# Performance work log

Measured on AMD Instinct MI355X. Metric: run time of the kernel, lower is better.

Reference implementation:

```python
import jax, jax.numpy as jnp
import numpy as np

FORGET_BIAS = 1.0  # TF LSTMCell default

def _lstm_step(c, h, x, W, b):
    # TF BasicLSTM/LSTMCell gate order: i, j (cell candidate), f, o
    z = jnp.concatenate([x, h], axis=-1) @ W + b
    i, j, f, o = jnp.split(z, 4, axis=-1)
    c_new = c * jax.nn.sigmoid(f + FORGET_BIAS) + jax.nn.sigmoid(i) * jnp.tanh(j)
    h_new = jnp.tanh(c_new) * jax.nn.sigmoid(o)
    return c_new, h_new

def setup_inputs() -> dict:
    key = jax.random.key(0)
    k1, k2, k3 = jax.random.split(key, 3)
    B, T, D, H1, H2 = 512, 2048, 1, 64, 1
    x = jax.random.normal(k1, (B, T, D), dtype=jnp.float32)
    W1 = jax.random.normal(k2, (D + H1, 4 * H1), dtype=jnp.float32) * 0.1
    b1 = jnp.zeros((4 * H1,), dtype=jnp.float32)
    W2 = jax.random.normal(k3, (H1 + H2, 4 * H2), dtype=jnp.float32) * 0.1
    b2 = jnp.zeros((4 * H2,), dtype=jnp.float32)
    return {"x": x, "W1": W1, "b1": b1, "W2": W2, "b2": b2}

def reference(x, W1, b1, W2, b2):
    B = x.shape[0]
    H1 = W1.shape[1] // 4
    H2 = W2.shape[1] // 4
    init = (jnp.zeros((B, H1), x.dtype), jnp.zeros((B, H1), x.dtype),
            jnp.zeros((B, H2), x.dtype), jnp.zeros((B, H2), x.dtype))

    def step(carry, x_t):
        c1, h1, c2, h2 = carry
        c1, h1 = _lstm_step(c1, h1, x_t, W1, b1)   # layer 1: LSTMCell(64)
        c2, h2 = _lstm_step(c2, h2, h1, W2, b2)    # layer 2: LSTMCell(1)
        return (c1, h1, c2, h2), h2

    xs = jnp.swapaxes(x, 0, 1)           # [T, B, 1]
    _, ys = jax.lax.scan(step, init, xs)  # ys: [T, B, 1]
    return jnp.swapaxes(ys, 0, 1)         # [B, T, 1]
```

## Files before the change

### kernel.cpp

```cpp
#include <hip/hip_runtime.h>

#define TT 2048

typedef float v2f __attribute__((ext_vector_type(2)));
typedef _Float16 h2v __attribute__((ext_vector_type(2)));

__device__ __forceinline__ v2f mk2(float a, float b) { v2f r; r.x = a; r.y = b; return r; }
__device__ __forceinline__ float rcpf(float x) { return __builtin_amdgcn_rcpf(x); }
__device__ __forceinline__ float fsig(float x) { return rcpf(1.0f + __expf(-x)); }
__device__ __forceinline__ float ftanh(float x) {
    return fmaf(2.0f, rcpf(1.0f + __expf(-2.0f * x)), -1.0f);
}

template<int C>
__device__ __forceinline__ float dppmov(float s) {
    return __int_as_float(__builtin_amdgcn_update_dpp(
        __float_as_int(s), __float_as_int(s), C, 0xF, 0xF, false));
}
template<int Q>
__device__ __forceinline__ float qbcast(float x) {
    return __int_as_float(__builtin_amdgcn_update_dpp(
        __float_as_int(x), __float_as_int(x), Q * 0x55, 0xF, 0xF, false));
}

#if __has_builtin(__builtin_amdgcn_fdot2)
#define DOT2(a, b, c) __builtin_amdgcn_fdot2((a), (b), (c), false)
#else
#define DOT2(a, b, c) fmaf((float)(a).x, (float)(b).x, \
                      fmaf((float)(a).y, (float)(b).y, (c)))
#endif

__device__ __forceinline__ h2v pk2(float a, float b) {
#if __has_builtin(__builtin_amdgcn_cvt_pkrtz)
    return __builtin_bit_cast(h2v, __builtin_amdgcn_cvt_pkrtz(a, b));
#else
    h2v r; r.x = (_Float16)a; r.y = (_Float16)b; return r;
#endif
}
__device__ __forceinline__ h2v bch(int v) { return __builtin_bit_cast(h2v, v); }

__global__ __launch_bounds__(64)
__attribute__((amdgpu_waves_per_eu(2, 2)))
void lstm1_f16(const float* __restrict__ x,
               const float* __restrict__ W1,
               const float* __restrict__ b1,
               const float* __restrict__ W2,
               float* __restrict__ zout)
{
    __shared__ __align__(16) float xall[TT];
    __shared__ __align__(16) _Float16 hring[16 * 72];
    __shared__ __align__(16) int wF4[8][64][4];
    __shared__ __align__(16) int wO4[8][64][4];
    __shared__ __align__(16) _Float16 w2lds[4][72];

    const int lane = threadIdx.x & 63;
    const int e    = blockIdx.x;
    const int u    = lane;

    for (int i = lane; i < TT; i += 64) xall[i] = x[(size_t)e * TT + i];
    for (int i = lane; i < 576; i += 64) ((int*)hring)[i] = 0;
    for (int kp = 0; kp < 32; ++kp) {
        wF4[kp >> 2][u][kp & 3] = __builtin_bit_cast(int,
            pk2(W1[(1 + 2*kp)*256 + 128 + u], W1[(2 + 2*kp)*256 + 128 + u]));
        wO4[kp >> 2][u][kp & 3] = __builtin_bit_cast(int,
            pk2(W1[(1 + 2*kp)*256 + 192 + u], W1[(2 + 2*kp)*256 + 192 + u]));
    }
    w2lds[0][lane] = (_Float16)W2[lane * 4 + 0];
    w2lds[1][lane] = (_Float16)W2[lane * 4 + 1];
    w2lds[2][lane] = (_Float16)W2[lane * 4 + 2];
    w2lds[3][lane] = (_Float16)W2[lane * 4 + 3];

#define DWQ(G, GO, q) \
    const h2v w##G##q##x = pk2(W1[(1+8*(q))*256 + (GO)*64 + u], W1[(2+8*(q))*256 + (GO)*64 + u]); \
    const h2v w##G##q##y = pk2(W1[(3+8*(q))*256 + (GO)*64 + u], W1[(4+8*(q))*256 + (GO)*64 + u]); \
    const h2v w##G##q##z = pk2(W1[(5+8*(q))*256 + (GO)*64 + u], W1[(6+8*(q))*256 + (GO)*64 + u]); \
    const h2v w##G##q##w = pk2(W1[(7+8*(q))*256 + (GO)*64 + u], W1[(8+8*(q))*256 + (GO)*64 + u]);
    DWQ(I, 0, 0) DWQ(I, 0, 1) DWQ(I, 0, 2) DWQ(I, 0, 3)
    DWQ(I, 0, 4) DWQ(I, 0, 5) DWQ(I, 0, 6) DWQ(I, 0, 7)
    DWQ(J, 1, 0) DWQ(J, 1, 1) DWQ(J, 1, 2) DWQ(J, 1, 3)
    DWQ(J, 1, 4) DWQ(J, 1, 5) DWQ(J, 1, 6) DWQ(J, 1, 7)
#undef DWQ

    const float w0I = W1[u],        bI = b1[u];
    const float w0J = W1[64 + u],   bJ = b1[64 + u];
    const float w0F = W1[128 + u],  bF = b1[128 + u] + 1.0f;
    const float w0O = W1[192 + u],  bO = b1[192 + u];

    const int tl = lane >> 2, gq = lane & 3;

    float c1 = 0.0f;
    __syncthreads();

    float* __restrict__ zb = zout + (size_t)e * TT * 4;
    const int* __restrict__ wFb = &wF4[0][0][0] + (u << 2);
    const int* __restrict__ wOb = &wO4[0][0][0] + (u << 2);

#define DGIJ(S, q, v) \
    accI##S = DOT2(bch((v).x), wI##q##x, accI##S); \
    accJ##S = DOT2(bch((v).x), wJ##q##x, accJ##S); \
    accI##S = DOT2(bch((v).y), wI##q##y, accI##S); \
    accJ##S = DOT2(bch((v).y), wJ##q##y, accJ##S); \
    accI##S = DOT2(bch((v).z), wI##q##z, accI##S); \
    accJ##S = DOT2(bch((v).z), wJ##q##z, accJ##S); \
    accI##S = DOT2(bch((v).w), wI##q##w, accI##S); \
    accJ##S = DOT2(bch((v).w), wJ##q##w, accJ##S);
#define FOD4(S, g, qv) { \
    const int4 wf_ = *(const int4*)(wFb + (g) * 256); \
    const int4 wo_ = *(const int4*)(wOb + (g) * 256); \
    accF##S = DOT2(bch((qv).x), bch(wf_.x), accF##S); \
    accO##S = DOT2(bch((qv).x), bch(wo_.x), accO##S); \
    accF##S = DOT2(bch((qv).y), bch(wf_.y), accF##S); \
    accO##S = DOT2(bch((qv).y), bch(wo_.y), accO##S); \
    accF##S = DOT2(bch((qv).z), bch(wf_.z), accF##S); \
    accO##S = DOT2(bch((qv).z), bch(wo_.z), accO##S); \
    accF##S = DOT2(bch((qv).w), bch(wf_.w), accF##S); \
    accO##S = DOT2(bch((qv).w), bch(wo_.w), accO##S); \
}

    for (int t = 0; t < TT; ++t) {
        const int4* hp = (const int4*)&hring[((t - 1) & 15) * 72];
        const int4 q0 = hp[0], q1 = hp[1], q2 = hp[2], q3 = hp[3];
        const int4 q4 = hp[4], q5 = hp[5], q6 = hp[6], q7 = hp[7];
        float accI0 = bI, accJ0 = bJ, accF0 = bF, accO0 = bO;
        float accI1 = 0.f, accJ1 = 0.f, accF1 = 0.f, accO1 = 0.f;
        DGIJ(0, 0, q0) DGIJ(1, 4, q4)
        DGIJ(0, 1, q1) DGIJ(1, 5, q5)
        DGIJ(0, 2, q2) DGIJ(1, 6, q6)
        DGIJ(0, 3, q3) DGIJ(1, 7, q7)
        FOD4(0, 0, q0) FOD4(1, 4, q4)
        FOD4(0, 1, q1) FOD4(1, 5, q5)
        FOD4(0, 2, q2) FOD4(1, 6, q6)
        FOD4(0, 3, q3) FOD4(1, 7, q7)
        const float xt = xall[t];
        const float zI = fmaf(xt, w0I, accI0 + accI1);
        const float zJ = fmaf(xt, w0J, accJ0 + accJ1);
        const float zF = fmaf(xt, w0F, accF0 + accF1);
        const float zO = fmaf(xt, w0O, accO0 + accO1);
        const float i_ = fsig(zI);
        const float j_ = ftanh(zJ);
        const float f_ = fsig(zF);
        const float o_ = fsig(zO);
        c1 = fmaf(c1, f_, i_ * j_);
        const float h1 = ftanh(c1) * o_;
        hring[(t & 15) * 72 + u] = (_Float16)h1;

        if ((t & 15) == 15) {
            const int4* hb  = (const int4*)&hring[tl * 72];
            const int4* w2q = (const int4*)&w2lds[gq][0];
            float z2 = 0.0f;
#pragma unroll
            for (int q = 0; q < 8; ++q) {
                const int4 wv = w2q[q];
                const int4 va = hb[q];
                z2 = DOT2(bch(va.x), bch(wv.x), z2);
                z2 = DOT2(bch(va.y), bch(wv.y), z2);
                z2 = DOT2(bch(va.z), bch(wv.z), z2);
                z2 = DOT2(bch(va.w), bch(wv.w), z2);
            }
            zb[(size_t)(t - 15 + tl) * 4 + gq] = z2;
        }
    }
#undef DGIJ
#undef FOD4
}

__global__ __launch_bounds__(64)
void lstm2_chain(const float* __restrict__ zp,
                 const float* __restrict__ W2,
                 const float* __restrict__ b2,
                 float* __restrict__ out)
{
    const int lane = threadIdx.x & 63;
    const int e    = lane >> 2;
    const int g    = lane & 3;
    const int elem = (blockIdx.x << 4) + e;

    const float w2h = W2[256 + g];
    const float bb  = b2[g] + ((g == 2) ? 1.0f : 0.0f);
    const float nlm = (g == 1) ? -2.0f : -1.0f;
    const float k2  = (g == 1) ?  2.0f :  1.0f;
    const float k3  = (g == 1) ? -1.0f :  0.0f;

    const float* __restrict__ zrow = zp + (size_t)elem * TT * 4 + g;
    float* __restrict__ orow = out + (size_t)elem * TT;

    float c2 = 0.0f, h2 = 0.0f;

    float zc[16];
#pragma unroll
    for (int k = 0; k < 16; ++k) zc[k] = zrow[k << 2];

    for (int t0 = 0; t0 < TT; t0 += 16) {
        float zn[16];
        if (t0 + 16 < TT) {
#pragma unroll
            for (int k = 0; k < 16; ++k) zn[k] = zrow[((t0 + 16 + k) << 2)];
        }
        float st0 = 0.f, st1 = 0.f, st2 = 0.f, st3 = 0.f;
#pragma unroll
        for (int k = 0; k < 16; ++k) {
            const float arg = fmaf(w2h, h2, zc[k] + bb);
            const float ev  = __expf(arg * nlm);
            const float rv  = rcpf(1.0f + ev);
            const float v   = fmaf(k2, rv, k3);
            const float vi = qbcast<0>(v), vj = qbcast<1>(v);
            const float vf = qbcast<2>(v), vo = qbcast<3>(v);
            c2 = fmaf(c2, vf, vi * vj);
            h2 = ftanh(c2) * vo;
            const bool mine = (g == (k & 3));
            if ((k >> 2) == 0) st0 = mine ? h2 : st0;
            else if ((k >> 2) == 1) st1 = mine ? h2 : st1;
            else if ((k >> 2) == 2) st2 = mine ? h2 : st2;
            else st3 = mine ? h2 : st3;
        }
        orow[t0 + g]      = st0;
        orow[t0 + 4 + g]  = st1;
        orow[t0 + 8 + g]  = st2;
        orow[t0 + 12 + g] = st3;
#pragma unroll
        for (int k = 0; k < 16; ++k) zc[k] = zn[k];
    }
}

__global__ __launch_bounds__(512)
__attribute__((amdgpu_waves_per_eu(4, 4)))
void lstm2_mono(const float* __restrict__ x,
                const float* __restrict__ W1,
                const float* __restrict__ b1,
                const float* __restrict__ W2,
                const float* __restrict__ b2,
                float* __restrict__ out)
{
    __shared__ __align__(16) float xall[TT + 4];
    __shared__ __align__(16) float h1x[2][80];
    __shared__ __align__(16) float zpq[4][4];
    __shared__ __align__(16) float h2buf[2][64];

    const int tid  = threadIdx.x;
    const int wave = tid >> 6;
    const int lane = tid & 63;
    const int b    = blockIdx.x;

    for (int i = tid; i < TT; i += 512) xall[i] = x[b * TT + i];
    if (tid < 4) xall[TT + tid] = 0.0f;

    const int u    = lane >> 3;
    const int h    = (lane >> 2) & 1;
    const int g    = lane & 3;
    const int unit = (wave << 3) + u;
    const int col  = (g << 6) + unit;

#define DECLW(k) const v2f wq##k = mk2(W1[(1 + 32*h + 2*(k)) * 256 + col], \
                                       W1[(2 + 32*h + 2*(k)) * 256 + col]);
    DECLW(0)  DECLW(1)  DECLW(2)  DECLW(3)
    DECLW(4)  DECLW(5)  DECLW(6)  DECLW(7)
    DECLW(8)  DECLW(9)  DECLW(10) DECLW(11)
    DECLW(12) DECLW(13) DECLW(14) DECLW(15)
#undef DECLW

    const float w0x   = (h == 0) ? W1[col] : 0.0f;
    const float biasF = (h == 0) ? (b1[col] + ((g == 2) ? 1.0f : 0.0f)) : 0.0f;
    const float nlm   = (g == 1) ? -2.0f : -1.0f;
    const bool  isj   = (g == 1);

    const float w2g  = W2[lane * 4 + (wave & 3)];
    const float w2h0 = W2[256], w2h1 = W2[257], w2h2 = W2[258], w2h3 = W2[259];
    const float b20 = b2[0], b21 = b2[1], b22 = b2[2], b23 = b2[3];

    float c1 = 0.0f;
    float c2 = 0.0f, h2v2 = 0.0f;

    const int hbase = h * 48;
    const int ridx  = lane + ((lane >> 5) << 4);
    const int widx  = (unit < 32) ? unit : unit + 16;

    if (tid < 160) ((float*)h1x)[tid] = 0.0f;
    __syncthreads();

    float* __restrict__ outb = out + b * TT;

#define WSUM(s) ({ float _s = (s);                                            \
    _s += dppmov<0x111>(_s); _s += dppmov<0x112>(_s); _s += dppmov<0x114>(_s);\
    _s += dppmov<0x118>(_s); _s += dppmov<0x142>(_s); _s += dppmov<0x143>(_s);\
    _s; })

#define STEP(P, t, xv)                                                        \
    {                                                                         \
        if ((t) < TT) {                                                       \
            const float4* hp = (const float4*)&h1x[P][hbase];                 \
            const float4 q0 = hp[0], q1 = hp[1], q2 = hp[2], q3 = hp[3];      \
            const float4 q4 = hp[4], q5 = hp[5], q6 = hp[6], q7 = hp[7];      \
            v2f a0 = mk2(fmaf((xv), w0x, biasF), 0.0f);                       \
            v2f a1 = mk2(0.f, 0.f), a2 = mk2(0.f, 0.f), a3 = mk2(0.f, 0.f);  \
            a0 = __builtin_elementwise_fma(mk2(q0.x, q0.y), wq0,  a0);        \
            a1 = __builtin_elementwise_fma(mk2(q0.z, q0.w), wq1,  a1);        \
            a2 = __builtin_elementwise_fma(mk2(q1.x, q1.y), wq2,  a2);        \
            a3 = __builtin_elementwise_fma(mk2(q1.z, q1.w), wq3,  a3);        \
            a0 = __builtin_elementwise_fma(mk2(q2.x, q2.y), wq4,  a0);        \
            a1 = __builtin_elementwise_fma(mk2(q2.z, q2.w), wq5,  a1);        \
            a2 = __builtin_elementwise_fma(mk2(q3.x, q3.y), wq6,  a2);        \
            a3 = __builtin_elementwise_fma(mk2(q3.z, q3.w), wq7,  a3);        \
            a0 = __builtin_elementwise_fma(mk2(q4.x, q4.y), wq8,  a0);        \
            a1 = __builtin_elementwise_fma(mk2(q4.z, q4.w), wq9,  a1);        \
            a2 = __builtin_elementwise_fma(mk2(q5.x, q5.y), wq10, a2);        \
            a3 = __builtin_elementwise_fma(mk2(q5.z, q5.w), wq11, a3);        \
            a0 = __builtin_elementwise_fma(mk2(q6.x, q6.y), wq12, a0);        \
            a1 = __builtin_elementwise_fma(mk2(q6.z, q6.w), wq13, a1);        \
            a2 = __builtin_elementwise_fma(mk2(q7.x, q7.y), wq14, a2);        \
            a3 = __builtin_elementwise_fma(mk2(q7.z, q7.w), wq15, a3);        \
            const v2f sv = (a0 + a1) + (a2 + a3);                             \
            const float zh = sv.x + sv.y;                                     \
            const float tshr = dppmov<0x114>(zh);                             \
            const float tshl = dppmov<0x104>(zh);                             \
            const float zfull = zh + (h ? tshr : tshl);                       \
            const float e = __expf(zfull * nlm);                              \
            const float r = rcpf(1.0f + e);                                   \
            const float v = isj ? fmaf(2.0f, r, -1.0f) : r;                   \
            const float gi = qbcast<0>(v), gj = qbcast<1>(v);                 \
            const float gf = qbcast<2>(v), go = qbcast<3>(v);                 \
            c1 = fmaf(c1, gf, gi * gj);                                       \
            const float h1v = ftanh(c1) * go;                                 \
            if ((lane & 7) == 0) h1x[(P) ^ 1][widx] = h1v;                    \
        }                                                                     \
        if (wave < 4 && (t) >= 1 && (t) <= TT) {                              \
            const float s = WSUM(h1x[P][ridx] * w2g);                         \
            if (lane == 63) zpq[((t) - 1) & 3][wave] = s;                     \
        }                                                                     \
        if (wave == 7 && lane == 0 && (t) >= 2 && (t) <= TT + 1) {            \
            const int st = (t) - 2;                                           \
            const float4 z4 = *(const float4*)zpq[st & 3];                    \
            const float zi = z4.x + fmaf(h2v2, w2h0, b20);                    \
            const float zj = z4.y + fmaf(h2v2, w2h1, b21);                    \
            const float zf = z4.z + fmaf(h2v2, w2h2, b22);                    \
            const float zo = z4.w + fmaf(h2v2, w2h3, b23);                    \
            c2 = c2 * fsig(zf + 1.0f) + fsig(zi) * ftanh(zj);                 \
            h2v2 = ftanh(c2) * fsig(zo);                                      \
            h2buf[(st >> 6) & 1][st & 63] = h2v2;                             \
        }                                                                     \
        __syncthreads();                                                      \
        if (wave == 4 && (t) >= 66 && ((t) & 63) == 2) {                      \
            const int blk = ((t) - 66) >> 6;                                  \
            outb[(blk << 6) + lane] = h2buf[blk & 1][lane];                   \
        }                                                                     \
    }

    for (int it = 0; it <= TT + 2; it += 2) {
        const float2 x2 = *(const float2*)&xall[it];
        STEP(0, it,     x2.x)
        STEP(1, it + 1, x2.y)
    }
#undef STEP
#undef WSUM
}

extern "C" void kernel_launch(void* const* d_in, const int* in_sizes, int n_in,
                              void* d_out, int out_size, void* d_ws, size_t ws_size,
                              hipStream_t stream)
{
    const float* x  = (const float*)d_in[0];
    const float* W1 = (const float*)d_in[1];
    const float* b1 = (const float*)d_in[2];
    const float* W2 = (const float*)d_in[3];
    const float* b2 = (const float*)d_in[4];
    float* out = (float*)d_out;

    const size_t need = (size_t)512 * TT * 4 * sizeof(float);
    if (ws_size >= need) {
        float* zp = (float*)d_ws;
        lstm1_f16<<<512, 64, 0, stream>>>(x, W1, b1, W2, zp);
        lstm2_chain<<<512 / 16, 64, 0, stream>>>(zp, W2, b2, out);
    } else {
        lstm2_mono<<<512, 512, 0, stream>>>(x, W1, b1, W2, b2, out);
    }
}
```

Measured before the change: 1.051 ms.

## Compute F/O gate recurrent dot products with MFMA, keep I/J on packed dot2

Moves the forget and output gate recurrent matvec (64x128) from per-lane fdot2 with LDS weight loads onto 16x16x32 f16 MFMA instructions. The weights are re-laid out in LDS as B fragments, and h is broadcast as the A operand, so only row 0 of each 16-row tile is useful. The I and J gates stay on register-resident fdot2. The waves-per-EU hint is also relaxed. The aim is to split the work between the matrix and vector units within each timestep. The cost is wasted MFMA rows, MFMA latency on the serial recurrence, and extra select logic to pick each lane's result.

```diff
diff --git a/kernel.cpp b/kernel.cpp
--- a/kernel.cpp
+++ b/kernel.cpp
@@ -4,6 +4,8 @@
 
 typedef float v2f __attribute__((ext_vector_type(2)));
 typedef _Float16 h2v __attribute__((ext_vector_type(2)));
+typedef _Float16 f16x8 __attribute__((ext_vector_type(8)));
+typedef float f32x4 __attribute__((ext_vector_type(4)));
 
 __device__ __forceinline__ v2f mk2(float a, float b) { v2f r; r.x = a; r.y = b; return r; }
 __device__ __forceinline__ float rcpf(float x) { return __builtin_amdgcn_rcpf(x); }
@@ -40,8 +42,8 @@
 __device__ __forceinline__ h2v bch(int v) { return __builtin_bit_cast(h2v, v); }
 
 __global__ __launch_bounds__(64)
-__attribute__((amdgpu_waves_per_eu(2, 2)))
-void lstm1_f16(const float* __restrict__ x,
+__attribute__((amdgpu_waves_per_eu(1)))
+void lstm1_hyb(const float* __restrict__ x,
                const float* __restrict__ W1,
                const float* __restrict__ b1,
                const float* __restrict__ W2,
@@ -49,22 +51,22 @@
 {
     __shared__ __align__(16) float xall[TT];
     __shared__ __align__(16) _Float16 hring[16 * 72];
-    __shared__ __align__(16) int wF4[8][64][4];
-    __shared__ __align__(16) int wO4[8][64][4];
+    __shared__ __align__(16) _Float16 wfo[2][8][64][8];
     __shared__ __align__(16) _Float16 w2lds[4][72];
 
     const int lane = threadIdx.x & 63;
     const int e    = blockIdx.x;
     const int u    = lane;
+    const int lg   = lane >> 4;
 
     for (int i = lane; i < TT; i += 64) xall[i] = x[(size_t)e * TT + i];
     for (int i = lane; i < 576; i += 64) ((int*)hring)[i] = 0;
-    for (int kp = 0; kp < 32; ++kp) {
-        wF4[kp >> 2][u][kp & 3] = __builtin_bit_cast(int,
-            pk2(W1[(1 + 2*kp)*256 + 128 + u], W1[(2 + 2*kp)*256 + 128 + u]));
-        wO4[kp >> 2][u][kp & 3] = __builtin_bit_cast(int,
-            pk2(W1[(1 + 2*kp)*256 + 192 + u], W1[(2 + 2*kp)*256 + 192 + u]));
-    }
+    for (int kt = 0; kt < 2; ++kt)
+        for (int n8 = 0; n8 < 8; ++n8)
+#pragma unroll
+            for (int j = 0; j < 8; ++j)
+                wfo[kt][n8][u][j] = (_Float16)
+                    W1[(size_t)(1 + kt*32 + (u >> 4)*8 + j) * 256 + 128 + 16*n8 + (u & 15)];
     w2lds[0][lane] = (_Float16)W2[lane * 4 + 0];
     w2lds[1][lane] = (_Float16)W2[lane * 4 + 1];
     w2lds[2][lane] = (_Float16)W2[lane * 4 + 2];
@@ -92,8 +94,7 @@
     __syncthreads();
 
     float* __restrict__ zb = zout + (size_t)e * TT * 4;
-    const int* __restrict__ wFb = &wF4[0][0][0] + (u << 2);
-    const int* __restrict__ wOb = &wO4[0][0][0] + (u << 2);
+    const f32x4 zf = {0.0f, 0.0f, 0.0f, 0.0f};
 
 #define DGIJ(S, q, v) \
     accI##S = DOT2(bch((v).x), wI##q##x, accI##S); \
@@ -104,40 +105,41 @@
     accJ##S = DOT2(bch((v).z), wJ##q##z, accJ##S); \
     accI##S = DOT2(bch((v).w), wI##q##w, accI##S); \
     accJ##S = DOT2(bch((v).w), wJ##q##w, accJ##S);
-#define FOD4(S, g, qv) { \
-    const int4 wf_ = *(const int4*)(wFb + (g) * 256); \
-    const int4 wo_ = *(const int4*)(wOb + (g) * 256); \
-    accF##S = DOT2(bch((qv).x), bch(wf_.x), accF##S); \
-    accO##S = DOT2(bch((qv).x), bch(wo_.x), accO##S); \
-    accF##S = DOT2(bch((qv).y), bch(wf_.y), accF##S); \
-    accO##S = DOT2(bch((qv).y), bch(wo_.y), accO##S); \
-    accF##S = DOT2(bch((qv).z), bch(wf_.z), accF##S); \
-    accO##S = DOT2(bch((qv).z), bch(wo_.z), accO##S); \
-    accF##S = DOT2(bch((qv).w), bch(wf_.w), accF##S); \
-    accO##S = DOT2(bch((qv).w), bch(wo_.w), accO##S); \
-}
+
+#define MM(a, b, c) __builtin_amdgcn_mfma_f32_16x16x32_f16((a), (b), (c), 0, 0, 0)
+#define LB(kt, n8) (*(const f16x8*)(&wfo[(kt)][(n8)][0][0] + (u << 3) + boff))
 
     for (int t = 0; t < TT; ++t) {
-        const int4* hp = (const int4*)&hring[((t - 1) & 15) * 72];
+        int boff = 0; asm volatile("" : "+v"(boff));
+        const int slot = ((t - 1) & 15) * 72;
+        const f16x8 A0 = *(const f16x8*)&hring[slot + lg * 8];
+        const f16x8 A1 = *(const f16x8*)&hring[slot + 32 + lg * 8];
+        const int4* hp = (const int4*)&hring[slot];
         const int4 q0 = hp[0], q1 = hp[1], q2 = hp[2], q3 = hp[3];
         const int4 q4 = hp[4], q5 = hp[5], q6 = hp[6], q7 = hp[7];
-        float accI0 = bI, accJ0 = bJ, accF0 = bF, accO0 = bO;
-        float accI1 = 0.f, accJ1 = 0.f, accF1 = 0.f, accO1 = 0.f;
+        f32x4 acF0 = MM(A0, LB(0,0), zf), acF1 = MM(A0, LB(0,1), zf);
+        f32x4 acF2 = MM(A0, LB(0,2), zf), acF3 = MM(A0, LB(0,3), zf);
+        f32x4 acO0 = MM(A0, LB(0,4), zf), acO1 = MM(A0, LB(0,5), zf);
+        f32x4 acO2 = MM(A0, LB(0,6), zf), acO3 = MM(A0, LB(0,7), zf);
+        acF0 = MM(A1, LB(1,0), acF0); acF1 = MM(A1, LB(1,1), acF1);
+        acF2 = MM(A1, LB(1,2), acF2); acF3 = MM(A1, LB(1,3), acF3);
+        acO0 = MM(A1, LB(1,4), acO0); acO1 = MM(A1, LB(1,5), acO1);
+        acO2 = MM(A1, LB(1,6), acO2); acO3 = MM(A1, LB(1,7), acO3);
+        float accI0 = bI, accJ0 = bJ;
+        float accI1 = 0.f, accJ1 = 0.f;
         DGIJ(0, 0, q0) DGIJ(1, 4, q4)
         DGIJ(0, 1, q1) DGIJ(1, 5, q5)
         DGIJ(0, 2, q2) DGIJ(1, 6, q6)
         DGIJ(0, 3, q3) DGIJ(1, 7, q7)
-        FOD4(0, 0, q0) FOD4(1, 4, q4)
-        FOD4(0, 1, q1) FOD4(1, 5, q5)
-        FOD4(0, 2, q2) FOD4(1, 6, q6)
-        FOD4(0, 3, q3) FOD4(1, 7, q7)
         const float xt = xall[t];
         const float zI = fmaf(xt, w0I, accI0 + accI1);
         const float zJ = fmaf(xt, w0J, accJ0 + accJ1);
-        const float zF = fmaf(xt, w0F, accF0 + accF1);
-        const float zO = fmaf(xt, w0O, accO0 + accO1);
         const float i_ = fsig(zI);
         const float j_ = ftanh(zJ);
+        const float zFs = (lg == 0) ? acF0.x : (lg == 1) ? acF1.x : (lg == 2) ? acF2.x : acF3.x;
+        const float zOs = (lg == 0) ? acO0.x : (lg == 1) ? acO1.x : (lg == 2) ? acO2.x : acO3.x;
+        const float zF = fmaf(xt, w0F, zFs + bF);
+        const float zO = fmaf(xt, w0O, zOs + bO);
         const float f_ = fsig(zF);
         const float o_ = fsig(zO);
         c1 = fmaf(c1, f_, i_ * j_);
@@ -161,7 +163,8 @@
         }
     }
 #undef DGIJ
-#undef FOD4
+#undef MM
+#undef LB
 }
 
 __global__ __launch_bounds__(64)
@@ -367,7 +370,7 @@
     const size_t need = (size_t)512 * TT * 4 * sizeof(float);
     if (ws_size >= need) {
         float* zp = (float*)d_ws;
-        lstm1_f16<<<512, 64, 0, stream>>>(x, W1, b1, W2, zp);
+        lstm1_hyb<<<512, 64, 0, stream>>>(x, W1, b1, W2, zp);
         lstm2_chain<<<512 / 16, 64, 0, stream>>>(zp, W2, b2, out);
     } else {
         lstm2_mono<<<512, 512, 0, stream>>>(x, W1, b1, W2, b2, out);
```

New measurement: 1.521 ms. 1.45x slower.
